# Kernel tuning notes

Hardware: AMD Instinct MI355X
Metric: run time of the kernel (lower is better)

The kernel has to match this reference:

```python
import jax, jax.numpy as jnp
import numpy as np


def _build_sparse_conv_problem():
    # Mirrors torchsparse rulebook construction for Conv3d(1,16,k=3,stride=2).
    rng = np.random.default_rng(0)
    B, R, N, Cin, Cout, S = 2, 512, 2_000_000, 1, 16, 2
    vol = R * R * R
    keys = np.unique(rng.integers(0, B * vol, size=int(N * 1.25), dtype=np.int64))[:N]
    b = keys // vol
    rem = keys % vol
    x = rem // (R * R)
    y = (rem // R) % R
    z = rem % R
    # output coords: unique floor-division by stride (torchsparse downsample)
    Ro = R // S
    ovol = Ro * Ro * Ro
    okeys = np.unique(((b * Ro + x // S) * Ro + (y // S)) * Ro + (z // S))
    n_out = int(okeys.shape[0])
    ob = okeys // ovol
    orem = okeys % ovol
    ox = orem // (Ro * Ro)
    oy = (orem // Ro) % Ro
    oz = orem % Ro
    # rulebook: for each of 27 offsets, find inputs at out*stride + offset
    in_list, out_list, k_list = [], [], []
    k = 0
    for dx in (-1, 0, 1):
        for dy in (-1, 0, 1):
            for dz in (-1, 0, 1):
                qx = ox * S + dx
                qy = oy * S + dy
                qz = oz * S + dz
                valid = (qx >= 0) & (qx < R) & (qy >= 0) & (qy < R) & (qz >= 0) & (qz < R)
                qkey = ((ob * R + qx) * R + qy) * R + qz
                pos = np.searchsorted(keys, qkey)
                pos = np.clip(pos, 0, N - 1)
                hit = valid & (keys[pos] == qkey)
                in_list.append(pos[hit].astype(np.int32))
                out_list.append(np.nonzero(hit)[0].astype(np.int32))
                k_list.append(np.full(int(hit.sum()), k, np.int32))
                k += 1
    in_idx = np.concatenate(in_list)
    out_idx = np.concatenate(out_list)
    k_idx = np.concatenate(k_list)
    return N, Cin, Cout, n_out, in_idx, out_idx, k_idx


def setup_inputs() -> dict:
    N, Cin, Cout, n_out, in_idx, out_idx, k_idx = _build_sparse_conv_problem()
    kf, kw = jax.random.split(jax.random.key(0))
    feats = jax.random.normal(kf, (N, Cin), dtype=jnp.float32)          # x.F
    weight = jax.random.normal(kw, (27, Cin, Cout), dtype=jnp.float32) * 0.1  # conv1 kernel
    return {
        "feats": feats,
        "weight": weight,
        "in_idx": jnp.asarray(in_idx),
        "out_idx": jnp.asarray(out_idx),
        "k_idx": jnp.asarray(k_idx),
        "n_out": n_out,
    }


def reference(feats, weight, in_idx, out_idx, k_idx, n_out):
    # gather-GEMM-scatter sparse 3D conv: out[o] += W[k] @ feats[i] for each
    # rulebook pair (i, o, k).
    gathered = feats[in_idx]                       # [M, Cin]
    contrib = jnp.einsum('mc,mco->mo', gathered, weight[k_idx])  # [M, Cout]
    return jax.ops.segment_sum(contrib, out_idx, num_segments=n_out)  # [n_out, Cout]
```

## Files before the change

kernel.cpp:

```cpp
#include <hip/hip_runtime.h>


typedef float vf4 __attribute__((ext_vector_type(4)));

__device__ inline unsigned short f32_to_bf16_rne(float x) {
    unsigned int u = __float_as_uint(x);
    unsigned int r = 0x7FFFu + ((u >> 16) & 1u);
    return (unsigned short)((u + r) >> 16);
}

__global__ void __launch_bounds__(256)
scatter_g(const float* __restrict__ feats,
          const int* __restrict__ in_idx,
          const int* __restrict__ out_idx,
          const int* __restrict__ k_idx,
          unsigned short* __restrict__ g,
          int M, int np) {
    int m = blockIdx.x * blockDim.x + threadIdx.x;
    if (m >= M) return;
    int i = in_idx[m];
    int o = out_idx[m];
    int k = k_idx[m];
    g[(size_t)k * np + o] = f32_to_bf16_rne(feats[i]);
}

__global__ void __launch_bounds__(256, 4)
reduce_g(const unsigned int* __restrict__ g32,
         const float* __restrict__ weight,
         float* __restrict__ out,
         int n_out, int half_np) {
    int t = blockIdx.x * blockDim.x + threadIdx.x;
    int o0 = t * 2;
    if (o0 >= n_out) return;

    unsigned int gu[27];
    #pragma unroll
    for (int k = 0; k < 27; ++k)
        gu[k] = g32[(size_t)k * half_np + t];

    vf4 a0 = {0,0,0,0}, a1 = a0, a2 = a0, a3 = a0;
    vf4 b0 = a0, b1 = a0, b2 = a0, b3 = a0;
    #pragma unroll
    for (int k = 0; k < 27; ++k) {
        const vf4* w = (const vf4*)&weight[k * 16];
        vf4 w0 = w[0], w1 = w[1], w2 = w[2], w3 = w[3];
        float fa = __uint_as_float(gu[k] << 16);
        float fb = __uint_as_float(gu[k] & 0xFFFF0000u);
        a0 += fa * w0; a1 += fa * w1; a2 += fa * w2; a3 += fa * w3;
        b0 += fb * w0; b1 += fb * w1; b2 += fb * w2; b3 += fb * w3;
    }

    vf4* op = (vf4*)(out + (size_t)o0 * 16);
    op[0] = a0; op[1] = a1; op[2] = a2; op[3] = a3;
    if (o0 + 1 < n_out) {
        op[4] = b0; op[5] = b1; op[6] = b2; op[7] = b3;
    }
}

__global__ void __launch_bounds__(256)
sparse_conv_scatter_atomic(const float* __restrict__ feats,
                           const float* __restrict__ weight,
                           const int* __restrict__ in_idx,
                           const int* __restrict__ out_idx,
                           const int* __restrict__ k_idx,
                           float* __restrict__ out,
                           int M) {
    long long t = (long long)blockIdx.x * blockDim.x + threadIdx.x;
    int m = (int)(t >> 4);
    int c = (int)(t & 15);
    if (m >= M) return;
    float f = feats[in_idx[m]];
    float w = weight[k_idx[m] * 16 + c];
    atomicAdd(out + (long long)out_idx[m] * 16 + c, f * w);
}

extern "C" void kernel_launch(void* const* d_in, const int* in_sizes, int n_in,
                              void* d_out, int out_size, void* d_ws, size_t ws_size,
                              hipStream_t stream) {
    const float* feats  = (const float*)d_in[0];
    const float* weight = (const float*)d_in[1];
    const int*   in_idx = (const int*)d_in[2];
    const int*   out_idx= (const int*)d_in[3];
    const int*   k_idx  = (const int*)d_in[4];
    float*       out    = (float*)d_out;

    const int M     = in_sizes[2];
    const int n_out = out_size / 16;
    const int np    = (n_out + 1) & ~1;

    const size_t need = (size_t)27 * (size_t)np * sizeof(unsigned short);
    const int block = 256;

    if (d_ws != nullptr && ws_size >= need) {
        unsigned short* g = (unsigned short*)d_ws;
        hipMemsetAsync(g, 0, need, stream);

        const int grid1 = (M + block - 1) / block;
        scatter_g<<<grid1, block, 0, stream>>>(feats, in_idx, out_idx, k_idx,
                                               g, M, np);

        const int nthr = (n_out + 1) / 2;
        const int grid2 = (nthr + block - 1) / block;
        reduce_g<<<grid2, block, 0, stream>>>((const unsigned int*)g, weight,
                                              out, n_out, np / 2);
    } else {
        hipMemsetAsync(d_out, 0, (size_t)out_size * sizeof(float), stream);
        const long long total = (long long)M * 16;
        const long long grid = (total + block - 1) / block;
        sparse_conv_scatter_atomic<<<(int)grid, block, 0, stream>>>(
            feats, weight, in_idx, out_idx, k_idx, out, M);
    }
}
```

Baseline: 234.6 us.

## Keep dense bf16 planes only for 8 parity offsets, atomically scatter the rest

Rulebook pairs are now split by kernel offset. The 8 offsets whose positive displacements match the stride-2 parity pattern stay in a dense bf16 workspace, now 8 planes instead of 27. A small 8-plane GEMV reduces that workspace. All remaining offsets go through a new per-pair kernel that issues 16 float atomicAdds into the output. This shrinks the workspace memset and the reduce-pass reads, but adds a second full pass over the index arrays and many millions of global atomics. The atomic adds also make the summation order nondeterministic.

```diff
diff --git a/kernel.cpp b/kernel.cpp
--- a/kernel.cpp
+++ b/kernel.cpp
@@ -9,43 +9,49 @@
     return (unsigned short)((u + r) >> 16);
 }
 
+__device__ inline int dense_plane(int k) {
+    int a = k / 9, b = (k / 3) % 3, c = k % 3;
+    if (a == 0 || b == 0 || c == 0) return -1;
+    return ((a - 1) << 2) | ((b - 1) << 1) | (c - 1);
+}
+
 __global__ void __launch_bounds__(256)
-scatter_g(const float* __restrict__ feats,
-          const int* __restrict__ in_idx,
-          const int* __restrict__ out_idx,
-          const int* __restrict__ k_idx,
-          unsigned short* __restrict__ g,
-          int M, int np) {
+scatter_dense(const float* __restrict__ feats,
+              const int* __restrict__ in_idx,
+              const int* __restrict__ out_idx,
+              const int* __restrict__ k_idx,
+              unsigned short* __restrict__ g,
+              int M, int np) {
     int m = blockIdx.x * blockDim.x + threadIdx.x;
     if (m >= M) return;
-    int i = in_idx[m];
-    int o = out_idx[m];
-    int k = k_idx[m];
-    g[(size_t)k * np + o] = f32_to_bf16_rne(feats[i]);
+    int p = dense_plane(k_idx[m]);
+    if (p < 0) return;
+    g[(size_t)p * np + out_idx[m]] = f32_to_bf16_rne(feats[in_idx[m]]);
 }
 
 __global__ void __launch_bounds__(256, 4)
-reduce_g(const unsigned int* __restrict__ g32,
-         const float* __restrict__ weight,
-         float* __restrict__ out,
-         int n_out, int half_np) {
+reduce8(const unsigned int* __restrict__ g32,
+        const float* __restrict__ weight,
+        float* __restrict__ out,
+        int n_out, int half_np) {
     int t = blockIdx.x * blockDim.x + threadIdx.x;
     int o0 = t * 2;
     if (o0 >= n_out) return;
 
-    unsigned int gu[27];
+    unsigned int gu[8];
     #pragma unroll
-    for (int k = 0; k < 27; ++k)
-        gu[k] = g32[(size_t)k * half_np + t];
+    for (int p = 0; p < 8; ++p)
+        gu[p] = g32[(size_t)p * half_np + t];
 
     vf4 a0 = {0,0,0,0}, a1 = a0, a2 = a0, a3 = a0;
     vf4 b0 = a0, b1 = a0, b2 = a0, b3 = a0;
+    const int KP[8] = {13, 14, 16, 17, 22, 23, 25, 26};
     #pragma unroll
-    for (int k = 0; k < 27; ++k) {
-        const vf4* w = (const vf4*)&weight[k * 16];
+    for (int p = 0; p < 8; ++p) {
+        const vf4* w = (const vf4*)&weight[KP[p] * 16];
         vf4 w0 = w[0], w1 = w[1], w2 = w[2], w3 = w[3];
-        float fa = __uint_as_float(gu[k] << 16);
-        float fb = __uint_as_float(gu[k] & 0xFFFF0000u);
+        float fa = __uint_as_float(gu[p] << 16);
+        float fb = __uint_as_float(gu[p] & 0xFFFF0000u);
         a0 += fa * w0; a1 += fa * w1; a2 += fa * w2; a3 += fa * w3;
         b0 += fb * w0; b1 += fb * w1; b2 += fb * w2; b3 += fb * w3;
     }
@@ -55,6 +61,26 @@
     if (o0 + 1 < n_out) {
         op[4] = b0; op[5] = b1; op[6] = b2; op[7] = b3;
     }
+}
+
+__global__ void __launch_bounds__(256)
+sparse_add(const float* __restrict__ feats,
+           const float* __restrict__ weight,
+           const int* __restrict__ in_idx,
+           const int* __restrict__ out_idx,
+           const int* __restrict__ k_idx,
+           float* __restrict__ out,
+           int M) {
+    int m = blockIdx.x * blockDim.x + threadIdx.x;
+    if (m >= M) return;
+    int k = k_idx[m];
+    if (dense_plane(k) >= 0) return;
+    float f = feats[in_idx[m]];
+    float* op = out + (long long)out_idx[m] * 16;
+    const float* w = &weight[k * 16];
+    #pragma unroll
+    for (int c = 0; c < 16; ++c)
+        atomicAdd(op + c, f * w[c]);
 }
 
 __global__ void __launch_bounds__(256)
@@ -88,7 +114,7 @@
     const int n_out = out_size / 16;
     const int np    = (n_out + 1) & ~1;
 
-    const size_t need = (size_t)27 * (size_t)np * sizeof(unsigned short);
+    const size_t need = (size_t)8 * (size_t)np * sizeof(unsigned short);
     const int block = 256;
 
     if (d_ws != nullptr && ws_size >= need) {
@@ -96,13 +122,16 @@
         hipMemsetAsync(g, 0, need, stream);
 
         const int grid1 = (M + block - 1) / block;
-        scatter_g<<<grid1, block, 0, stream>>>(feats, in_idx, out_idx, k_idx,
-                                               g, M, np);
+        scatter_dense<<<grid1, block, 0, stream>>>(feats, in_idx, out_idx,
+                                                   k_idx, g, M, np);
 
         const int nthr = (n_out + 1) / 2;
         const int grid2 = (nthr + block - 1) / block;
-        reduce_g<<<grid2, block, 0, stream>>>((const unsigned int*)g, weight,
-                                              out, n_out, np / 2);
+        reduce8<<<grid2, block, 0, stream>>>((const unsigned int*)g, weight,
+                                             out, n_out, np / 2);
+
+        sparse_add<<<grid1, block, 0, stream>>>(feats, weight, in_idx,
+                                                out_idx, k_idx, out, M);
     } else {
         hipMemsetAsync(d_out, 0, (size_t)out_size * sizeof(float), stream);
         const long long total = (long long)M * 16;
```

New measurement: 506.5 us. 116% more time.
